# Kernel tuning notes

Hardware: AMD Instinct MI355X
Metric: run time of the kernel (lower is better)

## Reference

```python
import jax, jax.numpy as jnp
import numpy as np

D_MODEL = 1024
N_HEAD = 16


def setup_inputs() -> dict:
    key = jax.random.key(0)
    ks = jax.random.split(key, 13)
    B, S, D = 2, 2048, D_MODEL
    scale = 1.0 / np.sqrt(D)
    inp = {
        "q": jax.random.normal(ks[0], (B, S, D), jnp.float32),
        "k": jax.random.normal(ks[1], (B, S, D), jnp.float32),
        "v": jax.random.normal(ks[2], (B, S, D), jnp.float32),
        "mask": jax.random.randint(ks[3], (1, 1, S, S), 0, 2, jnp.int32),
        "Wq": jax.random.normal(ks[4], (D, D), jnp.float32) * scale,
        "bq": jnp.zeros((D,), jnp.float32),
        "Wk": jax.random.normal(ks[5], (D, D), jnp.float32) * scale,
        "bk": jnp.zeros((D,), jnp.float32),
        "Wv": jax.random.normal(ks[6], (D, D), jnp.float32) * scale,
        "bv": jnp.zeros((D,), jnp.float32),
        "Wo": jax.random.normal(ks[7], (D, D), jnp.float32) * scale,
        "bo": jnp.zeros((D,), jnp.float32),
    }
    return inp


def _split_heads(x, n_head):
    # [B, S, D] -> [B, H, S, Dh]
    B, S, D = x.shape
    return x.reshape(B, S, n_head, D // n_head).transpose(0, 2, 1, 3)


def reference(q, k, v, mask, Wq, bq, Wk, bk, Wv, bv, Wo, bo):
    # linear projections (torch Linear: x @ W.T + b)
    qp = q @ Wq.T + bq
    kp = k @ Wk.T + bk
    vp = v @ Wv.T + bv
    qh = _split_heads(qp, N_HEAD)  # [B,H,S,Dh]
    kh = _split_heads(kp, N_HEAD)
    vh = _split_heads(vp, N_HEAD)
    d_k = qh.shape[-1]
    scores = jnp.einsum("bhqd,bhkd->bhqk", qh, kh) / jnp.sqrt(jnp.asarray(d_k, qh.dtype))
    neg = jnp.finfo(qh.dtype).min
    scores = jnp.where(mask == 0, neg, scores)
    attn = jax.nn.softmax(scores, axis=-1)
    out = jnp.einsum("bhqk,bhkd->bhqd", attn, vh)  # [B,H,S,Dh]
    B, H, S, Dh = out.shape
    concat = out.transpose(0, 2, 1, 3).reshape(B, S, H * Dh)
    return concat @ Wo.T + bo
```

## Files before the change

kernel.cpp:

```cpp
#include <hip/hip_runtime.h>
#include <hip/hip_bf16.h>

typedef __attribute__((ext_vector_type(8))) short short8;
typedef __attribute__((ext_vector_type(4))) float f32x4;
typedef __attribute__((ext_vector_type(4))) float floatv4;
typedef __attribute__((ext_vector_type(4))) unsigned int u32x4;
typedef unsigned short u16;
typedef unsigned int u32;
typedef unsigned long long u64;

#define S_LEN 2048
#define DMODEL 1024
#define NHEAD 16
#define DHEAD 64

__device__ __forceinline__ u16 f2bf(float f) {
  __hip_bfloat16 h = __float2bfloat16(f);
  return __builtin_bit_cast(u16, h);
}

__device__ __forceinline__ u32 cvtpk(float lo, float hi) {
  u32 r;
  asm("v_cvt_pk_bf16_f32 %0, %1, %2" : "=v"(r) : "v"(lo), "v"(hi));
  return r;
}

__device__ __forceinline__ void gload16(const void* g, void* l) {
  __builtin_amdgcn_global_load_lds(
      (const __attribute__((address_space(1))) u32*)g,
      (__attribute__((address_space(3))) u32*)l, 16, 0, 0);
}

__device__ __forceinline__ f32x4 mfma16(short8 a, short8 b, f32x4 c) {
  return __builtin_amdgcn_mfma_f32_16x16x32_bf16(a, b, c, 0, 0, 0);
}

__global__ void k_convert_qkv(const float* __restrict__ q, const float* __restrict__ k,
                              const float* __restrict__ v, u16* __restrict__ qb,
                              u16* __restrict__ kb, u16* __restrict__ vb) {
  const float* src = blockIdx.y == 0 ? q : blockIdx.y == 1 ? k : v;
  u16* dst = blockIdx.y == 0 ? qb : blockIdx.y == 1 ? kb : vb;
  int i = blockIdx.x * blockDim.x + threadIdx.x;
  floatv4 w = reinterpret_cast<const floatv4*>(src)[i];
  ushort4 o;
  o.x = f2bf(w.x); o.y = f2bf(w.y); o.z = f2bf(w.z); o.w = f2bf(w.w);
  reinterpret_cast<ushort4*>(dst)[i] = o;
}

__global__ void k_convert_w(const float* __restrict__ w0, const float* __restrict__ w1,
                            const float* __restrict__ w2, const float* __restrict__ w3,
                            u16* __restrict__ d0, u16* __restrict__ d1,
                            u16* __restrict__ d2, u16* __restrict__ d3) {
  const int z = blockIdx.y;
  const float* src = z == 0 ? w0 : z == 1 ? w1 : z == 2 ? w2 : w3;
  u16* dst = z == 0 ? d0 : z == 1 ? d1 : z == 2 ? d2 : d3;
  int i = blockIdx.x * blockDim.x + threadIdx.x;
  floatv4 w = reinterpret_cast<const floatv4*>(src)[i];
  ushort4 o;
  o.x = f2bf(w.x); o.y = f2bf(w.y); o.z = f2bf(w.z); o.w = f2bf(w.w);
  reinterpret_cast<ushort4*>(dst)[i] = o;
}

__global__ void k_maskpack(const int* __restrict__ mask, u64* __restrict__ bits) {
  int tid = blockIdx.x * blockDim.x + threadIdx.x;
  u64 b = __ballot(mask[tid] != 0);
  if ((threadIdx.x & 63) == 0) bits[tid >> 6] = b;
}

template <int BN>
__device__ __forceinline__ void gemm_body(const u16* __restrict__ A,
                                          const u16* __restrict__ W,
                                          const float* __restrict__ bias,
                                          void* __restrict__ dst, int mode) {
  constexpr int BM = 128, BK = 32, K = DMODEL;
  constexpr int MI = (BN == 128) ? 4 : 2;
  __shared__ u16 As[2][BM * BK];
  __shared__ u16 Bs[2][BN * BK];
  const int t = threadIdx.x;
  const int lane = t & 63, w = t >> 6;
  const int lr = lane & 15, lg = lane >> 4;
  const int wrow = (BN == 128) ? (w >> 1) * 64 : w * 32;
  const int wcol = (BN == 128) ? (w & 1) * 64 : 0;
  const int brow = blockIdx.y * BM, bcol = blockIdx.x * BN;

  const int sr = t >> 2, scg = (t & 3) * 8;
  const u16* Abase = A + (size_t)(brow + sr) * K + scg;
  const u16* Wbase = W + (size_t)(bcol + sr) * K + scg;

  f32x4 acc[MI][4] = {};

  auto stage = [&](int buf, int kt) {
    const int k0 = kt * BK;
    gload16(Abase + k0, &As[buf][w * 512]);
    gload16(Abase + (size_t)64 * K + k0, &As[buf][2048 + w * 512]);
    gload16(Wbase + k0, &Bs[buf][w * 512]);
    if constexpr (BN == 128)
      gload16(Wbase + (size_t)64 * K + k0, &Bs[buf][2048 + w * 512]);
  };

  stage(0, 0);
  __syncthreads();

  int cur = 0;
  constexpr int NT = K / BK;
  for (int kt = 0; kt < NT; ++kt) {
    if (kt + 1 < NT) stage(cur ^ 1, kt + 1);
    short8 af[MI], bfr[4];
#pragma unroll
    for (int i = 0; i < MI; ++i)
      af[i] = *(const short8*)&As[cur][(wrow + i * 16 + lr) * BK + lg * 8];
#pragma unroll
    for (int j = 0; j < 4; ++j)
      bfr[j] = *(const short8*)&Bs[cur][(wcol + j * 16 + lr) * BK + lg * 8];
#pragma unroll
    for (int i = 0; i < MI; ++i)
#pragma unroll
      for (int j = 0; j < 4; ++j)
        acc[i][j] = mfma16(af[i], bfr[j], acc[i][j]);
    __syncthreads();
    cur ^= 1;
  }

#pragma unroll
  for (int i = 0; i < MI; ++i) {
#pragma unroll
    for (int j = 0; j < 4; ++j) {
#pragma unroll
      for (int r = 0; r < 4; ++r) {
        const int m = brow + wrow + i * 16 + lg * 4 + r;
        const int n = bcol + wcol + j * 16 + lr;
        const float v = acc[i][j][r] + bias[n];
        if (mode == 0) {
          const int b = m >> 11, s = m & (S_LEN - 1), h = n >> 6, dh = n & 63;
          ((u16*)dst)[((size_t)(b * NHEAD + h) * S_LEN + s) * DHEAD + dh] = f2bf(v);
        } else if (mode == 1) {
          const int b = m >> 11, s = m & (S_LEN - 1), h = n >> 6, dh = n & 63;
          ((u16*)dst)[((size_t)(b * NHEAD + h) * DHEAD + dh) * S_LEN + s] = f2bf(v);
        } else {
          ((float*)dst)[(size_t)m * DMODEL + n] = v;
        }
      }
    }
  }
}

__global__ __launch_bounds__(256, 2) void k_gemm_qkv(
    const u16* __restrict__ qb, const u16* __restrict__ kb, const u16* __restrict__ vb,
    const u16* __restrict__ Wqb, const u16* __restrict__ Wkb, const u16* __restrict__ Wvb,
    const float* __restrict__ bq, const float* __restrict__ bk, const float* __restrict__ bv,
    u16* __restrict__ qh, u16* __restrict__ kh, u16* __restrict__ vT) {
  const int z = blockIdx.z;
  const u16* A = z == 0 ? qb : z == 1 ? kb : vb;
  const u16* W = z == 0 ? Wqb : z == 1 ? Wkb : Wvb;
  const float* b = z == 0 ? bq : z == 1 ? bk : bv;
  void* dst = z == 0 ? (void*)qh : z == 1 ? (void*)kh : (void*)vT;
  gemm_body<128>(A, W, b, dst, z == 2 ? 1 : 0);
}

__global__ __launch_bounds__(256, 2) void k_gemm_out(
    const u16* __restrict__ A, const u16* __restrict__ W,
    const float* __restrict__ bias, float* __restrict__ dst) {
  gemm_body<64>(A, W, bias, dst, 2);
}

__global__ __launch_bounds__(256, 4) void k_attn(
    const u16* __restrict__ Qh, const u16* __restrict__ Kh,
    const u16* __restrict__ Vt, const u64* __restrict__ Mb,
    u16* __restrict__ O) {
  constexpr int KB = 64;
  constexpr int NT = S_LEN / KB;
  __shared__ u16 Ks[2][KB * DHEAD];
  __shared__ u16 Vs[2][DHEAD * KB];
  const int t = threadIdx.x, lane = t & 63, w = t >> 6;
  const int lr = lane & 15, lg = lane >> 4;
  const int qt = blockIdx.x, bh = blockIdx.y;
  const size_t base = (size_t)bh * S_LEN * DHEAD;
  const int q0 = qt * 64;
  const int qrow = q0 + w * 16 + lr;

  short8 qf[2];
  {
    const u16* qp = Qh + base + (size_t)qrow * DHEAD + lg * 8;
    qf[0] = *(const short8*)qp;
    qf[1] = *(const short8*)(qp + 32);
  }

  f32x4 oacc[4] = {};
  float mrun = -1e30f, lrun = 0.f;

  const int sr = t >> 3;
  const int scg_k = (((t & 7) ^ (sr & 7)) * 8);
  const int scg_v = ((((t & 7) * 2) ^ (sr & 14)) * 4);

  auto stage = [&](int buf, int kt2) {
    const int kb0 = kt2 * KB;
    gload16(Kh + base + (size_t)(kb0 + sr) * DHEAD + scg_k, &Ks[buf][w * 512]);
    gload16(Kh + base + (size_t)(kb0 + 32 + sr) * DHEAD + scg_k, &Ks[buf][2048 + w * 512]);
    gload16(Vt + base + (size_t)sr * S_LEN + kb0 + scg_v, &Vs[buf][w * 512]);
    gload16(Vt + base + (size_t)(32 + sr) * S_LEN + kb0 + scg_v, &Vs[buf][2048 + w * 512]);
  };

  stage(0, 0);
  __syncthreads();

  const float SC = 0.125f * 1.44269504f;
  const int rsw = lr & 7;
  const int c0 = (lg ^ rsw) * 8, c1 = ((lg + 4) ^ rsw) * 8;

  int cur = 0;
  for (int kt2 = 0; kt2 < NT; ++kt2) {
    if (kt2 + 1 < NT) stage(cur ^ 1, kt2 + 1);
    u64 mw = Mb[(size_t)qrow * (S_LEN / 64) + kt2];

    f32x4 sc[4];
#pragma unroll
    for (int j = 0; j < 4; ++j) {
      f32x4 c = {};
      short8 k0 = *(const short8*)&Ks[cur][(j * 16 + lr) * 64 + c0];
      short8 k1 = *(const short8*)&Ks[cur][(j * 16 + lr) * 64 + c1];
      c = mfma16(k0, qf[0], c);
      c = mfma16(k1, qf[1], c);
      sc[j] = c;
    }

    const u32 mlo = (u32)(mw >> (lg * 4));
    const u32 mhi = (u32)(mw >> (32 + lg * 4));
#pragma unroll
    for (int j = 0; j < 4; ++j) {
      const u32 msrc = (j < 2) ? mlo : mhi;
      const int sh = (j & 1) * 16;
#pragma unroll
      for (int r = 0; r < 4; ++r) {
        float s = sc[j][r] * SC;
        sc[j][r] = ((msrc >> (sh + r)) & 1u) ? s : -1e30f;
      }
    }

    float pm;
    {
      float a0 = fmaxf(sc[0][0], sc[0][1]), a1 = fmaxf(sc[0][2], sc[0][3]);
      float a2 = fmaxf(sc[1][0], sc[1][1]), a3 = fmaxf(sc[1][2], sc[1][3]);
      float a4 = fmaxf(sc[2][0], sc[2][1]), a5 = fmaxf(sc[2][2], sc[2][3]);
      float a6 = fmaxf(sc[3][0], sc[3][1]), a7 = fmaxf(sc[3][2], sc[3][3]);
      float b0 = fmaxf(a0, a1), b1 = fmaxf(a2, a3), b2 = fmaxf(a4, a5), b3 = fmaxf(a6, a7);
      pm = fmaxf(fmaxf(b0, b1), fmaxf(b2, b3));
    }
    pm = fmaxf(pm, __shfl_xor(pm, 16));
    pm = fmaxf(pm, __shfl_xor(pm, 32));

    if (!__all(pm <= mrun + 8.0f)) {
      float mnew = fmaxf(mrun, pm);
      float alpha = exp2f(mrun - mnew);
      lrun *= alpha;
      mrun = mnew;
      float aC[4];
#pragma unroll
      for (int r = 0; r < 4; ++r) aC[r] = __shfl(alpha, lg * 4 + r);
#pragma unroll
      for (int jo = 0; jo < 4; ++jo)
#pragma unroll
        for (int r = 0; r < 4; ++r) oacc[jo][r] *= aC[r];
    }

#pragma unroll
    for (int j = 0; j < 4; ++j)
#pragma unroll
      for (int r = 0; r < 4; ++r) sc[j][r] = exp2f(sc[j][r] - mrun);
    float ps;
    {
      float a0 = sc[0][0] + sc[0][1], a1 = sc[0][2] + sc[0][3];
      float a2 = sc[1][0] + sc[1][1], a3 = sc[1][2] + sc[1][3];
      float a4 = sc[2][0] + sc[2][1], a5 = sc[2][2] + sc[2][3];
      float a6 = sc[3][0] + sc[3][1], a7 = sc[3][2] + sc[3][3];
      ps = ((a0 + a1) + (a2 + a3)) + ((a4 + a5) + (a6 + a7));
    }
    ps += __shfl_xor(ps, 16);
    ps += __shfl_xor(ps, 32);
    lrun += ps;

    u32x4 pa1 = {cvtpk(sc[0][0], sc[0][1]), cvtpk(sc[0][2], sc[0][3]),
                 cvtpk(sc[1][0], sc[1][1]), cvtpk(sc[1][2], sc[1][3])};
    u32x4 pa2 = {cvtpk(sc[2][0], sc[2][1]), cvtpk(sc[2][2], sc[2][3]),
                 cvtpk(sc[3][0], sc[3][1]), cvtpk(sc[3][2], sc[3][3])};
    short8 A1 = __builtin_bit_cast(short8, pa1);
    short8 A2 = __builtin_bit_cast(short8, pa2);

#pragma unroll
    for (int jo = 0; jo < 4; ++jo) {
      const int d = jo * 16 + lr;
      const u16* Vrow = &Vs[cur][d * 64];
      const int sw = d & 14;
      union { ushort4 h[2]; short8 s8; } vb1, vb2;
      vb1.h[0] = *(const ushort4*)&Vrow[((0 + lg) ^ sw) * 4];
      vb1.h[1] = *(const ushort4*)&Vrow[((4 + lg) ^ sw) * 4];
      vb2.h[0] = *(const ushort4*)&Vrow[((8 + lg) ^ sw) * 4];
      vb2.h[1] = *(const ushort4*)&Vrow[((12 + lg) ^ sw) * 4];
      oacc[jo] = mfma16(A1, vb1.s8, oacc[jo]);
      oacc[jo] = mfma16(A2, vb2.s8, oacc[jo]);
    }
    __syncthreads();
    cur ^= 1;
  }

  const int b = bh >> 4, h = bh & 15;
  const float invq = 1.0f / lrun;
  float inv[4];
#pragma unroll
  for (int r = 0; r < 4; ++r) inv[r] = __shfl(invq, lg * 4 + r);
#pragma unroll
  for (int jo = 0; jo < 4; ++jo)
#pragma unroll
    for (int r = 0; r < 4; ++r) {
      const int s = q0 + w * 16 + lg * 4 + r;
      const float o = oacc[jo][r] * inv[r];
      O[((size_t)(b * S_LEN + s)) * DMODEL + h * DHEAD + jo * 16 + lr] = f2bf(o);
    }
}

extern "C" void kernel_launch(void* const* d_in, const int* in_sizes, int n_in,
                              void* d_out, int out_size, void* d_ws, size_t ws_size,
                              hipStream_t stream) {
  const float* q = (const float*)d_in[0];
  const float* k = (const float*)d_in[1];
  const float* v = (const float*)d_in[2];
  const int* mask = (const int*)d_in[3];
  const float* Wq = (const float*)d_in[4];
  const float* bq = (const float*)d_in[5];
  const float* Wk = (const float*)d_in[6];
  const float* bk = (const float*)d_in[7];
  const float* Wv = (const float*)d_in[8];
  const float* bv = (const float*)d_in[9];
  const float* Wo = (const float*)d_in[10];
  const float* bo = (const float*)d_in[11];

  char* ws = (char*)d_ws;
  const size_t MB = 1024 * 1024;
  u16* qb  = (u16*)(ws + 0 * MB);
  u16* kb  = (u16*)(ws + 8 * MB);
  u16* vb  = (u16*)(ws + 16 * MB);
  u16* Wqb = (u16*)(ws + 24 * MB);
  u16* Wkb = (u16*)(ws + 26 * MB);
  u16* Wvb = (u16*)(ws + 28 * MB);
  u16* Wob = (u16*)(ws + 30 * MB);
  u16* qh  = (u16*)(ws + 32 * MB);
  u16* kh  = (u16*)(ws + 40 * MB);
  u16* vT  = (u16*)(ws + 48 * MB);
  u16* cc  = (u16*)(ws + 56 * MB);
  u64* mb  = (u64*)(ws + 64 * MB);

  k_convert_qkv<<<dim3(4096, 3), 256, 0, stream>>>(q, k, v, qb, kb, vb);
  k_convert_w<<<dim3(1024, 4), 256, 0, stream>>>(Wq, Wk, Wv, Wo, Wqb, Wkb, Wvb, Wob);
  k_maskpack<<<16384, 256, 0, stream>>>(mask, mb);

  k_gemm_qkv<<<dim3(8, 32, 3), 256, 0, stream>>>(qb, kb, vb, Wqb, Wkb, Wvb,
                                                 bq, bk, bv, qh, kh, vT);

  k_attn<<<dim3(S_LEN / 64, 32), 256, 0, stream>>>(qh, kh, vT, mb, cc);

  k_gemm_out<<<dim3(16, 32), 256, 0, stream>>>(cc, Wob, bo, (float*)d_out);
}
```

Before: 180.7 us.

## Fold softmax scale into Q projection and stage V through registers with padded LDS

Multiplies the Q projection output by the softmax scale (including log2e) in the GEMM epilogue, which removes the per-score multiply inside the attention loop. V tiles are now loaded from global memory into registers and written to a padded LDS buffer (row pitch 72) after the PV MFMAs, replacing the XOR-swizzled direct global-to-LDS loads. The mask word is also prefetched one iteration ahead. Rounding Q after scaling slightly changes bf16 rounding, and the register staging raises register pressure and adds LDS store work to each iteration.

```diff
diff --git a/kernel.cpp b/kernel.cpp
--- a/kernel.cpp
+++ b/kernel.cpp
@@ -71,7 +71,8 @@
 __device__ __forceinline__ void gemm_body(const u16* __restrict__ A,
                                           const u16* __restrict__ W,
                                           const float* __restrict__ bias,
-                                          void* __restrict__ dst, int mode) {
+                                          void* __restrict__ dst, int mode,
+                                          float scale) {
   constexpr int BM = 128, BK = 32, K = DMODEL;
   constexpr int MI = (BN == 128) ? 4 : 2;
   __shared__ u16 As[2][BM * BK];
@@ -129,7 +130,7 @@
       for (int r = 0; r < 4; ++r) {
         const int m = brow + wrow + i * 16 + lg * 4 + r;
         const int n = bcol + wcol + j * 16 + lr;
-        const float v = acc[i][j][r] + bias[n];
+        const float v = (acc[i][j][r] + bias[n]) * scale;
         if (mode == 0) {
           const int b = m >> 11, s = m & (S_LEN - 1), h = n >> 6, dh = n & 63;
           ((u16*)dst)[((size_t)(b * NHEAD + h) * S_LEN + s) * DHEAD + dh] = f2bf(v);
@@ -154,13 +155,14 @@
   const u16* W = z == 0 ? Wqb : z == 1 ? Wkb : Wvb;
   const float* b = z == 0 ? bq : z == 1 ? bk : bv;
   void* dst = z == 0 ? (void*)qh : z == 1 ? (void*)kh : (void*)vT;
-  gemm_body<128>(A, W, b, dst, z == 2 ? 1 : 0);
+  const float scale = z == 0 ? 0.125f * 1.44269504f : 1.0f;
+  gemm_body<128>(A, W, b, dst, z == 2 ? 1 : 0, scale);
 }
 
 __global__ __launch_bounds__(256, 2) void k_gemm_out(
     const u16* __restrict__ A, const u16* __restrict__ W,
     const float* __restrict__ bias, float* __restrict__ dst) {
-  gemm_body<64>(A, W, bias, dst, 2);
+  gemm_body<64>(A, W, bias, dst, 2, 1.0f);
 }
 
 __global__ __launch_bounds__(256, 4) void k_attn(
@@ -169,8 +171,9 @@
     u16* __restrict__ O) {
   constexpr int KB = 64;
   constexpr int NT = S_LEN / KB;
+  constexpr int VP = 72;
   __shared__ u16 Ks[2][KB * DHEAD];
-  __shared__ u16 Vs[2][DHEAD * KB];
+  __shared__ u16 Vs[2][DHEAD * VP];
   const int t = threadIdx.x, lane = t & 63, w = t >> 6;
   const int lr = lane & 15, lg = lane >> 4;
   const int qt = blockIdx.x, bh = blockIdx.y;
@@ -190,34 +193,45 @@
 
   const int sr = t >> 3;
   const int scg_k = (((t & 7) ^ (sr & 7)) * 8);
-  const int scg_v = ((((t & 7) * 2) ^ (sr & 14)) * 4);
-
-  auto stage = [&](int buf, int kt2) {
+  const int c8 = (t & 7) * 8;
+
+  auto stageK = [&](int buf, int kt2) {
     const int kb0 = kt2 * KB;
     gload16(Kh + base + (size_t)(kb0 + sr) * DHEAD + scg_k, &Ks[buf][w * 512]);
     gload16(Kh + base + (size_t)(kb0 + 32 + sr) * DHEAD + scg_k, &Ks[buf][2048 + w * 512]);
-    gload16(Vt + base + (size_t)sr * S_LEN + kb0 + scg_v, &Vs[buf][w * 512]);
-    gload16(Vt + base + (size_t)(32 + sr) * S_LEN + kb0 + scg_v, &Vs[buf][2048 + w * 512]);
   };
-
-  stage(0, 0);
+  const u16* vsrc0 = Vt + base + (size_t)sr * S_LEN + c8;
+  const u16* vsrc1 = Vt + base + (size_t)(sr + 32) * S_LEN + c8;
+
+  short8 va = *(const short8*)(vsrc0);
+  short8 vbr = *(const short8*)(vsrc1);
+  stageK(0, 0);
+  *(short8*)&Vs[0][sr * VP + c8] = va;
+  *(short8*)&Vs[0][(sr + 32) * VP + c8] = vbr;
   __syncthreads();
 
-  const float SC = 0.125f * 1.44269504f;
+  u64 mw_next = Mb[(size_t)qrow * (S_LEN / 64)];
+
   const int rsw = lr & 7;
-  const int c0 = (lg ^ rsw) * 8, c1 = ((lg + 4) ^ rsw) * 8;
+  const int kc0 = (lg ^ rsw) * 8, kc1 = ((lg + 4) ^ rsw) * 8;
 
   int cur = 0;
   for (int kt2 = 0; kt2 < NT; ++kt2) {
-    if (kt2 + 1 < NT) stage(cur ^ 1, kt2 + 1);
-    u64 mw = Mb[(size_t)qrow * (S_LEN / 64) + kt2];
+    const u64 mw = mw_next;
+    if (kt2 + 1 < NT) {
+      mw_next = Mb[(size_t)qrow * (S_LEN / 64) + kt2 + 1];
+      const int kb1 = (kt2 + 1) * KB;
+      va = *(const short8*)(vsrc0 + kb1);
+      vbr = *(const short8*)(vsrc1 + kb1);
+      stageK(cur ^ 1, kt2 + 1);
+    }
 
     f32x4 sc[4];
 #pragma unroll
     for (int j = 0; j < 4; ++j) {
       f32x4 c = {};
-      short8 k0 = *(const short8*)&Ks[cur][(j * 16 + lr) * 64 + c0];
-      short8 k1 = *(const short8*)&Ks[cur][(j * 16 + lr) * 64 + c1];
+      short8 k0 = *(const short8*)&Ks[cur][(j * 16 + lr) * 64 + kc0];
+      short8 k1 = *(const short8*)&Ks[cur][(j * 16 + lr) * 64 + kc1];
       c = mfma16(k0, qf[0], c);
       c = mfma16(k1, qf[1], c);
       sc[j] = c;
@@ -230,10 +244,8 @@
       const u32 msrc = (j < 2) ? mlo : mhi;
       const int sh = (j & 1) * 16;
 #pragma unroll
-      for (int r = 0; r < 4; ++r) {
-        float s = sc[j][r] * SC;
-        sc[j][r] = ((msrc >> (sh + r)) & 1u) ? s : -1e30f;
-      }
+      for (int r = 0; r < 4; ++r)
+        sc[j][r] = ((msrc >> (sh + r)) & 1u) ? sc[j][r] : -1e30f;
     }
 
     float pm;
@@ -287,16 +299,19 @@
 
 #pragma unroll
     for (int jo = 0; jo < 4; ++jo) {
-      const int d = jo * 16 + lr;
-      const u16* Vrow = &Vs[cur][d * 64];
-      const int sw = d & 14;
+      const u16* Vrow = &Vs[cur][(jo * 16 + lr) * VP + lg * 4];
       union { ushort4 h[2]; short8 s8; } vb1, vb2;
-      vb1.h[0] = *(const ushort4*)&Vrow[((0 + lg) ^ sw) * 4];
-      vb1.h[1] = *(const ushort4*)&Vrow[((4 + lg) ^ sw) * 4];
-      vb2.h[0] = *(const ushort4*)&Vrow[((8 + lg) ^ sw) * 4];
-      vb2.h[1] = *(const ushort4*)&Vrow[((12 + lg) ^ sw) * 4];
+      vb1.h[0] = *(const ushort4*)&Vrow[0];
+      vb1.h[1] = *(const ushort4*)&Vrow[16];
+      vb2.h[0] = *(const ushort4*)&Vrow[32];
+      vb2.h[1] = *(const ushort4*)&Vrow[48];
       oacc[jo] = mfma16(A1, vb1.s8, oacc[jo]);
       oacc[jo] = mfma16(A2, vb2.s8, oacc[jo]);
+    }
+
+    if (kt2 + 1 < NT) {
+      *(short8*)&Vs[cur ^ 1][sr * VP + c8] = va;
+      *(short8*)&Vs[cur ^ 1][(sr + 32) * VP + c8] = vbr;
     }
     __syncthreads();
     cur ^= 1;
```

After: 178.3 us. No clear change (-1.3%).
